# Kernel optimization log

Measured on AMD Instinct MI355X. Metric: run time of the kernel, lower is better.

Reference implementation:

```python
import jax, jax.numpy as jnp
import numpy as np

BN_EPS = 1e-5
NORM_EPS = 1e-12  # F.normalize default eps


def reference(x, conv_w, bn_gamma, bn_beta):
    # 1x1 conv dimension reduction: [B,2048,H,W] -> [B,256,H,W]
    z = jnp.einsum('bchw,dc->bdhw', x, conv_w)
    # BatchNorm2d (training-mode batch statistics) + ReLU
    mu = z.mean(axis=(0, 2, 3), keepdims=True)
    var = z.var(axis=(0, 2, 3), keepdims=True)
    z = (z - mu) / jnp.sqrt(var + BN_EPS)
    z = z * bn_gamma.reshape(1, -1, 1, 1) + bn_beta.reshape(1, -1, 1, 1)
    z = jax.nn.relu(z)

    B, d, h, w = z.shape
    M = h * w
    xm = z.reshape(B, d, M)
    # Covpool: y = x I_hat x^T with I_hat = (I - 11^T/M)/M == centered 2nd moment
    xc = xm - xm.mean(axis=-1, keepdims=True)
    cov = jnp.einsum('bdm,bem->bde', xc, xc) / M  # [B,d,d]

    # Eigen decomposition (cov is symmetric PSD; SVD of PSD == eigh)
    s, U = jnp.linalg.eigh(cov)  # s: [B,d], U: [B,d,d]
    eps = jnp.finfo(cov.dtype).eps
    s = jnp.maximum(s, eps)

    # ExponentialInverse: U exp(-S) U^T
    inv_x = jnp.einsum('bid,bd,bjd->bij', U, jnp.exp(-s), U)
    # Power (matrix sqrt): U S^{1/2} U^T
    out = jnp.einsum('bid,bd,bjd->bij', U, jnp.sqrt(s), U)

    # attention = out @ inv_x^T  (inv_x is symmetric, transpose kept for fidelity)
    att = jnp.einsum('bij,bkj->bik', out, inv_x)
    flat = att.reshape(B, -1)
    nrm = jnp.maximum(jnp.linalg.norm(flat, axis=1, keepdims=True), NORM_EPS)
    normalized = (flat / nrm).reshape(att.shape)
    att = out * (att / normalized)

    y = att + out
    iu = jnp.triu_indices(d)
    return y[:, iu[0], iu[1]]  # [B, d*(d+1)/2]


def setup_inputs() -> dict:
    key = jax.random.key(0)
    k1, k2 = jax.random.split(key)
    x = jax.random.normal(k1, (32, 2048, 28, 28), dtype=jnp.float32)
    # kaiming-normal fan_out scaling for 1x1 conv: std = sqrt(2/fan_out)=sqrt(2/256)
    conv_w = jax.random.normal(k2, (256, 2048), dtype=jnp.float32) * np.sqrt(2.0 / 256.0)
    bn_gamma = jnp.ones((256,), dtype=jnp.float32)
    bn_beta = jnp.zeros((256,), dtype=jnp.float32)
    return {'x': x, 'conv_w': conv_w, 'bn_gamma': bn_gamma, 'bn_beta': bn_beta}
```

## Files before the change

kernel.cpp:

```cpp
#include <hip/hip_runtime.h>


typedef unsigned short u16;
typedef __attribute__((ext_vector_type(8))) short bf16x8;
typedef __attribute__((ext_vector_type(4))) float f32x4;

__device__ __forceinline__ u16 f2bf(float f) {
  unsigned u = __builtin_bit_cast(unsigned, f);
  u += 0x7FFFu + ((u >> 16) & 1u);
  return (u16)(u >> 16);
}
__device__ __forceinline__ float bf2f(u16 h) {
  unsigned u = ((unsigned)h) << 16;
  return __builtin_bit_cast(float, u);
}

__device__ __forceinline__
void mm_core(const u16* __restrict__ Ah, const u16* __restrict__ Al,
             const u16* __restrict__ Bh, const u16* __restrict__ Bl,
             long boff, int row0, int col0,
             u16 (*lds)[128][8][8], f32x4 acc[4][4])
{
  const int tid = threadIdx.x;
  const int wave = tid >> 6, lane = tid & 63;
  const int wm = wave >> 1, wn = wave & 1;
  const int mL = lane & 15, q = lane >> 4;
  const u16* baseA[2] = {Ah + boff, Al + boff};
  const u16* baseB[2] = {Bh + boff, Bl + boff};

  for (int k0 = 0; k0 < 256; k0 += 64) {
    __syncthreads();
#pragma unroll
    for (int it = 0; it < 16; ++it) {
      const int t = it >> 2;
      const int r = ((it & 3) << 8) + tid;
      const int m = r >> 3, c = r & 7;
      const u16* src = (t < 2 ? baseA[t] : baseB[t - 2])
                     + (long)((t < 2 ? row0 : col0) + m) * 256 + k0 + c * 8;
      const uint4 v = *reinterpret_cast<const uint4*>(src);
      *reinterpret_cast<uint4*>(&lds[t][m][c ^ (m & 7)][0]) = v;
    }
    __syncthreads();
#pragma unroll
    for (int kk = 0; kk < 2; ++kk) {
      bf16x8 ah[4], al[4], bh[4], bl[4];
#pragma unroll
      for (int i = 0; i < 4; ++i) {
        const int ma = wm * 64 + i * 16 + mL;
        const int ca = (kk * 4 + q) ^ (ma & 7);
        ah[i] = *reinterpret_cast<const bf16x8*>(&lds[0][ma][ca][0]);
        al[i] = *reinterpret_cast<const bf16x8*>(&lds[1][ma][ca][0]);
        const int nb = wn * 64 + i * 16 + mL;
        const int cb = (kk * 4 + q) ^ (nb & 7);
        bh[i] = *reinterpret_cast<const bf16x8*>(&lds[2][nb][cb][0]);
        bl[i] = *reinterpret_cast<const bf16x8*>(&lds[3][nb][cb][0]);
      }
#pragma unroll
      for (int i = 0; i < 4; ++i)
#pragma unroll
        for (int j = 0; j < 4; ++j) {
          acc[i][j] = __builtin_amdgcn_mfma_f32_16x16x32_bf16(ah[i], bh[j], acc[i][j], 0, 0, 0);
          acc[i][j] = __builtin_amdgcn_mfma_f32_16x16x32_bf16(ah[i], bl[j], acc[i][j], 0, 0, 0);
          acc[i][j] = __builtin_amdgcn_mfma_f32_16x16x32_bf16(al[i], bh[j], acc[i][j], 0, 0, 0);
        }
    }
  }
}

template<int MODE>
__global__ __launch_bounds__(256)
void gemm2_k(const u16* __restrict__ Ah, const u16* __restrict__ Al,
             const u16* __restrict__ Bh, const u16* __restrict__ Bl,
             u16* __restrict__ Ch, u16* __restrict__ Cl,
             u16* __restrict__ Dh, u16* __restrict__ Dl,
             const float* __restrict__ covf,
             float alpha, float b1, float diag, float* __restrict__ attn2)
{
  __shared__ u16 lds[4][128][8][8];
  const long boff = (long)blockIdx.z * 65536;
  const int row0 = blockIdx.y * 128, col0 = blockIdx.x * 128;
  const int wave = threadIdx.x >> 6, lane = threadIdx.x & 63;
  const int wm = wave >> 1, wn = wave & 1;
  const int mL = lane & 15, q = lane >> 4;

  f32x4 acc[4][4];
#pragma unroll
  for (int i = 0; i < 4; ++i)
#pragma unroll
    for (int j = 0; j < 4; ++j) acc[i][j] = {0.f, 0.f, 0.f, 0.f};

  mm_core(Ah, Al, Bh, Bl, boff, row0, col0, lds, acc);

  if (MODE == 2) {
    float ssum = 0.f;
#pragma unroll
    for (int i = 0; i < 4; ++i)
#pragma unroll
      for (int j = 0; j < 4; ++j)
#pragma unroll
        for (int rg = 0; rg < 4; ++rg) ssum = fmaf(acc[i][j][rg], acc[i][j][rg], ssum);
#pragma unroll
    for (int o = 32; o > 0; o >>= 1) ssum += __shfl_down(ssum, o);
    __syncthreads();
    float* red = (float*)&lds[0][0][0][0];
    if (lane == 0) red[wave] = ssum;
    __syncthreads();
    if (threadIdx.x == 0)
      atomicAdd(attn2 + blockIdx.z, red[0] + red[1] + red[2] + red[3]);
    return;
  }

#pragma unroll
  for (int i = 0; i < 4; ++i) {
    const int rbase = row0 + wm * 64 + i * 16 + q * 4;
#pragma unroll
    for (int j = 0; j < 4; ++j) {
      const int cc = col0 + wn * 64 + j * 16 + mL;
#pragma unroll
      for (int rg = 0; rg < 4; ++rg) {
        const int rr = rbase + rg;
        const long o = boff + (long)rr * 256 + cc;
        if (MODE == 0) {
          float v = alpha * acc[i][j][rg];
          if (covf) v = fmaf(b1, covf[o], v);
          if (rr == cc) v += diag;
          const u16 h = f2bf(v);
          Ch[o] = h; Cl[o] = f2bf(v - bf2f(h));
        } else {
          const float v = acc[i][j][rg];
          u16 h = f2bf(v);
          Ch[o] = h; Cl[o] = f2bf(v - bf2f(h));
          float hv = v * (1.f / 40320.f) - covf[o] * (1.f / 5040.f);
          if (rr == cc) hv += 1.f / 720.f;
          h = f2bf(hv);
          Dh[o] = h; Dl[o] = f2bf(hv - bf2f(h));
        }
      }
    }
  }
}

__global__ __launch_bounds__(256)
void gemm2_pair_k(const u16* __restrict__ A0, const u16* __restrict__ B0, u16* __restrict__ C0,
                  const u16* __restrict__ A1, const u16* __restrict__ B1, u16* __restrict__ C1,
                  long LO)
{
  __shared__ u16 lds[4][128][8][8];
  int z = blockIdx.z;
  const u16 *Ah, *Bh; u16* Chp;
  if (z < 32) { Ah = A0; Bh = B0; Chp = C0; }
  else { z -= 32; Ah = A1; Bh = B1; Chp = C1; }
  const long boff = (long)z * 65536;
  const int row0 = blockIdx.y * 128, col0 = blockIdx.x * 128;
  const int wave = threadIdx.x >> 6, lane = threadIdx.x & 63;
  const int wm = wave >> 1, wn = wave & 1;
  const int mL = lane & 15, q = lane >> 4;

  f32x4 acc[4][4];
#pragma unroll
  for (int i = 0; i < 4; ++i)
#pragma unroll
    for (int j = 0; j < 4; ++j) acc[i][j] = {0.f, 0.f, 0.f, 0.f};

  mm_core(Ah, Ah + LO, Bh, Bh + LO, boff, row0, col0, lds, acc);

#pragma unroll
  for (int i = 0; i < 4; ++i) {
    const int rbase = row0 + wm * 64 + i * 16 + q * 4;
#pragma unroll
    for (int j = 0; j < 4; ++j) {
      const int cc = col0 + wn * 64 + j * 16 + mL;
#pragma unroll
      for (int rg = 0; rg < 4; ++rg) {
        const long o = boff + (long)(rbase + rg) * 256 + cc;
        const float v = acc[i][j][rg];
        const u16 h = f2bf(v);
        Chp[o] = h; Chp[o + LO] = f2bf(v - bf2f(h));
      }
    }
  }
}

__global__ __launch_bounds__(512)
void conv_k(const u16* __restrict__ wb, const float* __restrict__ x,
            float* __restrict__ z)
{
  __shared__ u16 ldsA[256][8][8];
  __shared__ u16 ldsB[128][8][8];
  const int tid = threadIdx.x;
  const int b = blockIdx.z;
  const int n0 = blockIdx.x * 128;
  const int wave = tid >> 6, lane = tid & 63;
  const int wm = wave >> 1, wn = wave & 1;
  const int mL = lane & 15, q = lane >> 4;
  const float* xb = x + (long)b * 2048 * 784;

  f32x4 acc[4][4];
#pragma unroll
  for (int i = 0; i < 4; ++i)
#pragma unroll
    for (int j = 0; j < 4; ++j) acc[i][j] = {0.f, 0.f, 0.f, 0.f};

  for (int k0 = 0; k0 < 2048; k0 += 64) {
    __syncthreads();
#pragma unroll
    for (int it = 0; it < 4; ++it) {
      const int g = it * 512 + tid;
      const int m = g >> 3, c = g & 7;
      const uint4 v = *reinterpret_cast<const uint4*>(wb + (long)m * 2048 + k0 + c * 8);
      *reinterpret_cast<uint4*>(&ldsA[m][c ^ (m & 7)][0]) = v;
    }
    {
      const int kg = tid >> 5, nc = tid & 31;
      const int kbase = kg * 4, nbase = nc * 4;
      float vv[4][4];
#pragma unroll
      for (int jk = 0; jk < 4; ++jk) {
        const int gk = k0 + kbase + jk;
        const int gn = n0 + nbase;
        float4 f = make_float4(0.f, 0.f, 0.f, 0.f);
        if (gn < 784) f = *reinterpret_cast<const float4*>(xb + (long)gk * 784 + gn);
        vv[jk][0] = f.x; vv[jk][1] = f.y; vv[jk][2] = f.z; vv[jk][3] = f.w;
      }
      const int c = kbase >> 3, ko = kbase & 7;
#pragma unroll
      for (int jn = 0; jn < 4; ++jn) {
        const int n = nbase + jn;
        ushort4 u;
        u.x = f2bf(vv[0][jn]); u.y = f2bf(vv[1][jn]);
        u.z = f2bf(vv[2][jn]); u.w = f2bf(vv[3][jn]);
        *reinterpret_cast<ushort4*>(&ldsB[n][c ^ (n & 7)][ko]) = u;
      }
    }
    __syncthreads();
#pragma unroll
    for (int kk = 0; kk < 2; ++kk) {
      bf16x8 af[4], bfv[4];
#pragma unroll
      for (int i = 0; i < 4; ++i) {
        const int ma = wm * 64 + i * 16 + mL;
        af[i] = *reinterpret_cast<const bf16x8*>(&ldsA[ma][(kk * 4 + q) ^ (ma & 7)][0]);
        const int nb = wn * 64 + i * 16 + mL;
        bfv[i] = *reinterpret_cast<const bf16x8*>(&ldsB[nb][(kk * 4 + q) ^ (nb & 7)][0]);
      }
#pragma unroll
      for (int i = 0; i < 4; ++i)
#pragma unroll
        for (int j = 0; j < 4; ++j)
          acc[i][j] = __builtin_amdgcn_mfma_f32_16x16x32_bf16(af[i], bfv[j], acc[i][j], 0, 0, 0);
    }
  }
#pragma unroll
  for (int i = 0; i < 4; ++i) {
    const int rbase = wm * 64 + i * 16 + q * 4;
#pragma unroll
    for (int j = 0; j < 4; ++j) {
      const int cc = n0 + wn * 64 + j * 16 + mL;
      if (cc >= 784) continue;
#pragma unroll
      for (int rg = 0; rg < 4; ++rg)
        z[((long)b * 256 + rbase + rg) * 784 + cc] = acc[i][j][rg];
    }
  }
}

__global__ __launch_bounds__(256)
void gram_k(const u16* __restrict__ zb, const float* __restrict__ rs,
            float* __restrict__ cov)
{
  __shared__ u16 lds[2][128][8][8];
  const int tid = threadIdx.x;
  const int b = blockIdx.z;
  const int col0 = blockIdx.x * 128, row0 = blockIdx.y * 128;
  const int wave = tid >> 6, lane = tid & 63;
  const int wm = wave >> 1, wn = wave & 1;
  const int mL = lane & 15, q = lane >> 4;
  const u16* zbb = zb + (long)b * 256 * 832;

  f32x4 acc[4][4];
#pragma unroll
  for (int i = 0; i < 4; ++i)
#pragma unroll
    for (int j = 0; j < 4; ++j) acc[i][j] = {0.f, 0.f, 0.f, 0.f};

  for (int k0 = 0; k0 < 832; k0 += 64) {
    __syncthreads();
#pragma unroll
    for (int it = 0; it < 8; ++it) {
      const int t = it >> 2;
      const int r = ((it & 3) << 8) + tid;
      const int m = r >> 3, c = r & 7;
      const int grow = (t == 0 ? row0 : col0) + m;
      const uint4 v = *reinterpret_cast<const uint4*>(zbb + (long)grow * 832 + k0 + c * 8);
      *reinterpret_cast<uint4*>(&lds[t][m][c ^ (m & 7)][0]) = v;
    }
    __syncthreads();
#pragma unroll
    for (int kk = 0; kk < 2; ++kk) {
      bf16x8 af[4], bfv[4];
#pragma unroll
      for (int i = 0; i < 4; ++i) {
        const int ma = wm * 64 + i * 16 + mL;
        af[i] = *reinterpret_cast<const bf16x8*>(&lds[0][ma][(kk * 4 + q) ^ (ma & 7)][0]);
        const int nb = wn * 64 + i * 16 + mL;
        bfv[i] = *reinterpret_cast<const bf16x8*>(&lds[1][nb][(kk * 4 + q) ^ (nb & 7)][0]);
      }
#pragma unroll
      for (int i = 0; i < 4; ++i)
#pragma unroll
        for (int j = 0; j < 4; ++j)
          acc[i][j] = __builtin_amdgcn_mfma_f32_16x16x32_bf16(af[i], bfv[j], acc[i][j], 0, 0, 0);
    }
  }
  const float inv_m = 1.f / 784.f;
#pragma unroll
  for (int i = 0; i < 4; ++i) {
    const int rr0 = row0 + wm * 64 + i * 16 + q * 4;
#pragma unroll
    for (int j = 0; j < 4; ++j) {
      const int cc = col0 + wn * 64 + j * 16 + mL;
      const float mu_c = rs[b * 256 + cc] * inv_m;
#pragma unroll
      for (int rg = 0; rg < 4; ++rg) {
        const int rr = rr0 + rg;
        const float mu_r = rs[b * 256 + rr] * inv_m;
        cov[((long)b * 256 + rr) * 256 + cc] = fmaf(acc[i][j][rg], inv_m, -mu_r * mu_c);
      }
    }
  }
}

__global__ __launch_bounds__(256)
void bn_fuse_k(const float* __restrict__ z, const float* __restrict__ gamma,
               const float* __restrict__ beta, u16* __restrict__ zb,
               float* __restrict__ rs)
{
  const int d = blockIdx.x, t = threadIdx.x;
  const int lane = t & 63, wid = t >> 6;
  __shared__ float ws[4], wq[4], bc[2];

  float s = 0.f, qq = 0.f;
  for (int b = 0; b < 32; ++b) {
    const float* p = z + ((long)b * 256 + d) * 784;
    for (int m = t; m < 784; m += 256) {
      const float v = p[m];
      s += v; qq = fmaf(v, v, qq);
    }
  }
#pragma unroll
  for (int o = 32; o > 0; o >>= 1) { s += __shfl_down(s, o); qq += __shfl_down(qq, o); }
  if (lane == 0) { ws[wid] = s; wq[wid] = qq; }
  __syncthreads();
  if (t == 0) {
    const float inv_n = 1.f / 25088.f;
    const float sum = ws[0] + ws[1] + ws[2] + ws[3];
    const float sq  = wq[0] + wq[1] + wq[2] + wq[3];
    const float mean = sum * inv_n;
    const float var  = sq * inv_n - mean * mean;
    const float sc = gamma[d] * rsqrtf(var + 1e-5f);
    bc[0] = sc; bc[1] = fmaf(-mean, sc, beta[d]);
  }
  __syncthreads();
  const float sc = bc[0], sh = bc[1];

  for (int b = 0; b < 32; ++b) {
    const float* p = z + ((long)b * 256 + d) * 784;
    u16* qp = zb + ((long)b * 256 + d) * 832;
    float rsum = 0.f;
    for (int m = t; m < 832; m += 256) {
      const float v = (m < 784) ? fmaxf(fmaf(p[m], sc, sh), 0.f) : 0.f;
      qp[m] = f2bf(v);
      rsum += v;
    }
#pragma unroll
    for (int o = 32; o > 0; o >>= 1) rsum += __shfl_down(rsum, o);
    if (lane == 0) ws[wid] = rsum;
    __syncthreads();
    if (t == 0) rs[b * 256 + d] = ws[0] + ws[1] + ws[2] + ws[3];
    __syncthreads();
  }
}

__global__ __launch_bounds__(256)
void power_k(const float* __restrict__ cov, float* __restrict__ s,
             float* __restrict__ attn2)
{
  const int b = blockIdx.x, i = threadIdx.x;
  const float* A = cov + (long)b * 65536;
  __shared__ float v[256];
  __shared__ float red[4];
  v[i] = 1.f;
  __syncthreads();
  float lam = 1.f;
  for (int it = 0; it < 10; ++it) {
    float u = 0.f;
#pragma unroll 8
    for (int j = 0; j < 256; ++j) u = fmaf(A[(long)j * 256 + i], v[j], u);
    float ss = u * u;
#pragma unroll
    for (int o = 32; o > 0; o >>= 1) ss += __shfl_down(ss, o);
    if ((i & 63) == 0) red[i >> 6] = ss;
    __syncthreads();
    lam = sqrtf(red[0] + red[1] + red[2] + red[3]);
    v[i] = u / lam;
    __syncthreads();
  }
  if (i == 0) { s[b] = 1.8f / lam; attn2[b] = 0.f; }
}

__global__ __launch_bounds__(256)
void init_k(const float* __restrict__ cov, const float* __restrict__ s,
            u16* __restrict__ Yh, u16* __restrict__ Yl,
            u16* __restrict__ Th, u16* __restrict__ Tl)
{
  const int b = blockIdx.y, i = blockIdx.x, j = threadIdx.x;
  const long o = ((long)b * 256 + i) * 256 + j;
  const float a = cov[o] * s[b];
  u16 h = f2bf(a);
  Yh[o] = h; Yl[o] = f2bf(a - bf2f(h));
  float tv = -0.5f * a;
  if (i == j) tv += 1.5f;
  h = f2bf(tv);
  Th[o] = h; Tl[o] = f2bf(tv - bf2f(h));
}

__global__ __launch_bounds__(256)
void split_cov_k(const float* __restrict__ cov, u16* __restrict__ Ch, u16* __restrict__ Cl)
{
  const int b = blockIdx.y, i = blockIdx.x, j = threadIdx.x;
  const long o = ((long)b * 256 + i) * 256 + j;
  const float a = cov[o];
  const u16 h = f2bf(a);
  Ch[o] = h; Cl[o] = f2bf(a - bf2f(h));
}

__global__ __launch_bounds__(256)
void out_k(const u16* __restrict__ Yh, const u16* __restrict__ Yl,
           const float* __restrict__ s, const float* __restrict__ attn2,
           float* __restrict__ out)
{
  const int i = blockIdx.x, b = blockIdx.y, j = threadIdx.x;
  if (j < i) return;
  const float inv = rsqrtf(s[b]);
  const float nrm = fmaxf(sqrtf(fmaxf(attn2[b], 0.f)) * inv, 1e-12f);
  const float scv = inv * (1.f + nrm);
  const long o = ((long)b * 256 + i) * 256 + j;
  const long off = (long)b * 32896 + (long)i * 256 - (long)i * (i - 1) / 2 + (j - i);
  out[off] = (bf2f(Yh[o]) + bf2f(Yl[o])) * scv;
}

__global__ __launch_bounds__(256)
void cast_w_k(const float* __restrict__ w, u16* __restrict__ wb)
{
  const int idx = blockIdx.x * 256 + threadIdx.x;
  wb[idx] = f2bf(w[idx]);
}

extern "C" void kernel_launch(void* const* d_in, const int* in_sizes, int n_in,
                              void* d_out, int out_size, void* d_ws, size_t ws_size,
                              hipStream_t stream)
{
  const float* x     = (const float*)d_in[0];
  const float* w     = (const float*)d_in[1];
  const float* gamma = (const float*)d_in[2];
  const float* beta  = (const float*)d_in[3];
  float* out = (float*)d_out;

  const long PS = 4194304;
  const long LO = 2097152;
  u16* S[5];
  for (int k = 0; k < 5; ++k) S[k] = (u16*)d_ws + (long)k * PS;
  float* z   = (float*)d_ws;
  u16*   zb  = (u16*)((char*)d_ws + 25690112);
  float* cov = (float*)((char*)d_ws + 41943040);
  u16*   wb  = (u16*)((char*)d_ws + 41943040);
  float* st  = (float*)((char*)d_ws + 50331648);
  float* sv = st, *attn2 = st + 32, *rs = st + 64;

  const dim3 blk(256);
  const dim3 gM(2, 2, 32);
  const dim3 gP(2, 2, 64);
  const dim3 gE(256, 32);

  auto G0 = [&](const u16* A_, const u16* B_, u16* C_, const float* Pf,
                float alpha, float b1, float diag) {
    gemm2_k<0><<<gM, blk, 0, stream>>>(A_, A_ + LO, B_, B_ + LO, C_, C_ + LO,
                                       (u16*)nullptr, (u16*)nullptr, Pf,
                                       alpha, b1, diag, (float*)nullptr);
  };

  cast_w_k<<<dim3(2048), blk, 0, stream>>>(w, wb);
  conv_k<<<dim3(7, 1, 32), dim3(512), 0, stream>>>(wb, x, z);
  bn_fuse_k<<<dim3(256), blk, 0, stream>>>(z, gamma, beta, zb, rs);
  gram_k<<<gM, blk, 0, stream>>>(zb, rs, cov);
  power_k<<<dim3(32), blk, 0, stream>>>(cov, sv, attn2);
  init_k<<<gE, blk, 0, stream>>>(cov, sv, S[0], S[0] + LO, S[1], S[1] + LO);
  G0(S[0], S[1], S[2], nullptr, 1.f, 0.f, 0.f);

  int iY = 2, iZ = 1, fa = 0, fb = 3, fc = 4;
  for (int it = 1; it <= 7; ++it) {
    const int iT = fa;
    G0(S[iZ], S[iY], S[iT], nullptr, -0.5f, 0.f, 1.5f);
    if (it < 7) {
      gemm2_pair_k<<<gP, blk, 0, stream>>>(S[iY], S[iT], S[fb],
                                           S[iT], S[iZ], S[fc], LO);
      const int nY = fb, nZ = fc;
      fa = iY; fb = iZ; fc = iT;
      iY = nY; iZ = nZ;
    } else {
      G0(S[iY], S[iT], S[fb], nullptr, 1.f, 0.f, 0.f);
      iY = fb;
    }
  }
  int fr[4], nf = 0;
  for (int k = 0; k < 5; ++k) if (k != iY) fr[nf++] = k;
  u16* C2 = S[fr[0]]; u16* V = S[fr[1]]; u16* Ha = S[fr[2]]; u16* Hb = S[fr[3]];

  split_cov_k<<<gE, blk, 0, stream>>>(cov, C2, C2 + LO);
  gemm2_k<1><<<gM, blk, 0, stream>>>(C2, C2 + LO, C2, C2 + LO, V, V + LO,
                                     Ha, Ha + LO, cov, 1.f, 0.f, 0.f, (float*)nullptr);
  G0(V, Ha, Hb, cov, 1.f, -1.f / 120.f, 1.f / 24.f);
  G0(V, Hb, Ha, cov, 1.f, -1.f / 6.f,   0.5f);
  G0(V, Ha, Hb, cov, 1.f, -1.f,         1.f);

  gemm2_k<2><<<gM, blk, 0, stream>>>(S[iY], S[iY] + LO, Hb, Hb + LO,
                                     (u16*)nullptr, (u16*)nullptr,
                                     (u16*)nullptr, (u16*)nullptr,
                                     (const float*)nullptr, 1.f, 0.f, 0.f, attn2);
  out_k<<<gE, blk, 0, stream>>>(S[iY], S[iY] + LO, sv, attn2, out);
}
```

Before: 819.4 us.

## Co-schedule exp-polynomial GEMMs with Newton-Schulz steps and split BN into parallel kernels

Moves the Taylor-series matrix-exponential GEMM chain into the same launches as the first Newton-Schulz iterations, so independent 32-batch GEMMs share one 64-block grid instead of running as separate small grids. It also fuses the weight bf16 cast into the conv loader and the cov hi/lo split into the gram epilogue. BatchNorm is split into a stats kernel and an apply kernel with much wider grids. Remaining standalone GEMMs use a 128x64 tile to double the block count. The cost is extra workspace buffers and more launches in the BN path.

Result: faster. 776.2 us (-5.3%).

```diff
diff --git a/kernel.cpp b/kernel.cpp
--- a/kernel.cpp
+++ b/kernel.cpp
@@ -67,17 +67,22 @@
   }
 }
 
-template<int MODE>
-__global__ __launch_bounds__(256)
-void gemm2_k(const u16* __restrict__ Ah, const u16* __restrict__ Al,
-             const u16* __restrict__ Bh, const u16* __restrict__ Bl,
-             u16* __restrict__ Ch, u16* __restrict__ Cl,
-             u16* __restrict__ Dh, u16* __restrict__ Dl,
-             const float* __restrict__ covf,
-             float alpha, float b1, float diag, float* __restrict__ attn2)
+template<int MB>
+__global__ __launch_bounds__(256)
+void fuse_k(const u16* __restrict__ A0, const u16* __restrict__ B0, u16* __restrict__ C0,
+            float al0, float b10, float dg0, const float* __restrict__ cf0,
+            const u16* __restrict__ A1, const u16* __restrict__ B1, u16* __restrict__ C1,
+            u16* __restrict__ D1, float al1, float b11, float dg1,
+            float hc1, float hc2, float hc3, const float* __restrict__ cf1, long LO)
 {
   __shared__ u16 lds[4][128][8][8];
-  const long boff = (long)blockIdx.z * 65536;
+  int z = blockIdx.z;
+  const bool hB = (z >= 32);
+  const u16 *Ah, *Bh; u16 *C, *D = nullptr;
+  float al, b1, dg; const float* cf;
+  if (!hB) { Ah = A0; Bh = B0; C = C0; al = al0; b1 = b10; dg = dg0; cf = cf0; }
+  else { z -= 32; Ah = A1; Bh = B1; C = C1; D = D1; al = al1; b1 = b11; dg = dg1; cf = cf1; }
+  const long boff = (long)z * 65536;
   const int row0 = blockIdx.y * 128, col0 = blockIdx.x * 128;
   const int wave = threadIdx.x >> 6, lane = threadIdx.x & 63;
   const int wm = wave >> 1, wn = wave & 1;
@@ -89,26 +94,7 @@
 #pragma unroll
     for (int j = 0; j < 4; ++j) acc[i][j] = {0.f, 0.f, 0.f, 0.f};
 
-  mm_core(Ah, Al, Bh, Bl, boff, row0, col0, lds, acc);
-
-  if (MODE == 2) {
-    float ssum = 0.f;
-#pragma unroll
-    for (int i = 0; i < 4; ++i)
-#pragma unroll
-      for (int j = 0; j < 4; ++j)
-#pragma unroll
-        for (int rg = 0; rg < 4; ++rg) ssum = fmaf(acc[i][j][rg], acc[i][j][rg], ssum);
-#pragma unroll
-    for (int o = 32; o > 0; o >>= 1) ssum += __shfl_down(ssum, o);
-    __syncthreads();
-    float* red = (float*)&lds[0][0][0][0];
-    if (lane == 0) red[wave] = ssum;
-    __syncthreads();
-    if (threadIdx.x == 0)
-      atomicAdd(attn2 + blockIdx.z, red[0] + red[1] + red[2] + red[3]);
-    return;
-  }
+  mm_core(Ah, Ah + LO, Bh, Bh + LO, boff, row0, col0, lds, acc);
 
 #pragma unroll
   for (int i = 0; i < 4; ++i) {
@@ -120,20 +106,20 @@
       for (int rg = 0; rg < 4; ++rg) {
         const int rr = rbase + rg;
         const long o = boff + (long)rr * 256 + cc;
-        if (MODE == 0) {
-          float v = alpha * acc[i][j][rg];
-          if (covf) v = fmaf(b1, covf[o], v);
-          if (rr == cc) v += diag;
+        const float vr = acc[i][j][rg];
+        if (MB == 1 && hB) {
+          u16 h = f2bf(vr);
+          C[o] = h; C[o + LO] = f2bf(vr - bf2f(h));
+          float hv = fmaf(vr, hc1, cf[o] * hc2);
+          if (rr == cc) hv += hc3;
+          h = f2bf(hv);
+          D[o] = h; D[o + LO] = f2bf(hv - bf2f(h));
+        } else {
+          float v = al * vr;
+          if (cf) v = fmaf(b1, cf[o], v);
+          if (rr == cc) v += dg;
           const u16 h = f2bf(v);
-          Ch[o] = h; Cl[o] = f2bf(v - bf2f(h));
-        } else {
-          const float v = acc[i][j][rg];
-          u16 h = f2bf(v);
-          Ch[o] = h; Cl[o] = f2bf(v - bf2f(h));
-          float hv = v * (1.f / 40320.f) - covf[o] * (1.f / 5040.f);
-          if (rr == cc) hv += 1.f / 720.f;
-          h = f2bf(hv);
-          Dh[o] = h; Dl[o] = f2bf(hv - bf2f(h));
+          C[o] = h; C[o + LO] = f2bf(v - bf2f(h));
         }
       }
     }
@@ -181,8 +167,121 @@
   }
 }
 
+template<int MODE>
+__global__ __launch_bounds__(256)
+void gemmN64_k(const u16* __restrict__ Ah, const u16* __restrict__ Al,
+               const u16* __restrict__ Bh, const u16* __restrict__ Bl,
+               u16* __restrict__ Ch, u16* __restrict__ Cl,
+               const float* __restrict__ cf, float alpha, float b1, float diag,
+               float* __restrict__ attn2)
+{
+  __shared__ u16 ldsA[2][128][8][8];
+  __shared__ u16 ldsB[2][64][8][8];
+  const long boff = (long)blockIdx.z * 65536;
+  const int row0 = blockIdx.y * 128, col0 = blockIdx.x * 64;
+  const int tid = threadIdx.x;
+  const int wave = tid >> 6, lane = tid & 63;
+  const int wm = wave >> 1, wn = wave & 1;
+  const int mL = lane & 15, q = lane >> 4;
+  const u16* baseA[2] = {Ah + boff, Al + boff};
+  const u16* baseB[2] = {Bh + boff, Bl + boff};
+
+  f32x4 acc[4][2];
+#pragma unroll
+  for (int i = 0; i < 4; ++i)
+#pragma unroll
+    for (int j = 0; j < 2; ++j) acc[i][j] = {0.f, 0.f, 0.f, 0.f};
+
+  for (int k0 = 0; k0 < 256; k0 += 64) {
+    __syncthreads();
+#pragma unroll
+    for (int it = 0; it < 8; ++it) {
+      const int t = it >> 2;
+      const int r = ((it & 3) << 8) + tid;
+      const int m = r >> 3, c = r & 7;
+      const uint4 v = *reinterpret_cast<const uint4*>(
+          baseA[t] + (long)(row0 + m) * 256 + k0 + c * 8);
+      *reinterpret_cast<uint4*>(&ldsA[t][m][c ^ (m & 7)][0]) = v;
+    }
+#pragma unroll
+    for (int it = 0; it < 4; ++it) {
+      const int t = it >> 1;
+      const int r = ((it & 1) << 8) + tid;
+      const int m = r >> 3, c = r & 7;
+      const uint4 v = *reinterpret_cast<const uint4*>(
+          baseB[t] + (long)(col0 + m) * 256 + k0 + c * 8);
+      *reinterpret_cast<uint4*>(&ldsB[t][m][c ^ (m & 7)][0]) = v;
+    }
+    __syncthreads();
+#pragma unroll
+    for (int kk = 0; kk < 2; ++kk) {
+      bf16x8 ah[4], alo[4], bh[2], bl[2];
+#pragma unroll
+      for (int i = 0; i < 4; ++i) {
+        const int ma = wm * 64 + i * 16 + mL;
+        const int ca = (kk * 4 + q) ^ (ma & 7);
+        ah[i]  = *reinterpret_cast<const bf16x8*>(&ldsA[0][ma][ca][0]);
+        alo[i] = *reinterpret_cast<const bf16x8*>(&ldsA[1][ma][ca][0]);
+      }
+#pragma unroll
+      for (int j = 0; j < 2; ++j) {
+        const int nb = wn * 32 + j * 16 + mL;
+        const int cb = (kk * 4 + q) ^ (nb & 7);
+        bh[j] = *reinterpret_cast<const bf16x8*>(&ldsB[0][nb][cb][0]);
+        bl[j] = *reinterpret_cast<const bf16x8*>(&ldsB[1][nb][cb][0]);
+      }
+#pragma unroll
+      for (int i = 0; i < 4; ++i)
+#pragma unroll
+        for (int j = 0; j < 2; ++j) {
+          acc[i][j] = __builtin_amdgcn_mfma_f32_16x16x32_bf16(ah[i],  bh[j], acc[i][j], 0, 0, 0);
+          acc[i][j] = __builtin_amdgcn_mfma_f32_16x16x32_bf16(ah[i],  bl[j], acc[i][j], 0, 0, 0);
+          acc[i][j] = __builtin_amdgcn_mfma_f32_16x16x32_bf16(alo[i], bh[j], acc[i][j], 0, 0, 0);
+        }
+    }
+  }
+
+  if (MODE == 2) {
+    float ssum = 0.f;
+#pragma unroll
+    for (int i = 0; i < 4; ++i)
+#pragma unroll
+      for (int j = 0; j < 2; ++j)
+#pragma unroll
+        for (int rg = 0; rg < 4; ++rg) ssum = fmaf(acc[i][j][rg], acc[i][j][rg], ssum);
+#pragma unroll
+    for (int o = 32; o > 0; o >>= 1) ssum += __shfl_down(ssum, o);
+    __syncthreads();
+    float* red = (float*)&ldsA[0][0][0][0];
+    if (lane == 0) red[wave] = ssum;
+    __syncthreads();
+    if (tid == 0)
+      atomicAdd(attn2 + blockIdx.z, red[0] + red[1] + red[2] + red[3]);
+    return;
+  }
+
+#pragma unroll
+  for (int i = 0; i < 4; ++i) {
+    const int rbase = row0 + wm * 64 + i * 16 + q * 4;
+#pragma unroll
+    for (int j = 0; j < 2; ++j) {
+      const int cc = col0 + wn * 32 + j * 16 + mL;
+#pragma unroll
+      for (int rg = 0; rg < 4; ++rg) {
+        const int rr = rbase + rg;
+        const long o = boff + (long)rr * 256 + cc;
+        float v = alpha * acc[i][j][rg];
+        if (cf) v = fmaf(b1, cf[o], v);
+        if (rr == cc) v += diag;
+        const u16 h = f2bf(v);
+        Ch[o] = h; Cl[o] = f2bf(v - bf2f(h));
+      }
+    }
+  }
+}
+
 __global__ __launch_bounds__(512)
-void conv_k(const u16* __restrict__ wb, const float* __restrict__ x,
+void conv_k(const float* __restrict__ w, const float* __restrict__ x,
             float* __restrict__ z)
 {
   __shared__ u16 ldsA[256][8][8];
@@ -207,8 +306,13 @@
     for (int it = 0; it < 4; ++it) {
       const int g = it * 512 + tid;
       const int m = g >> 3, c = g & 7;
-      const uint4 v = *reinterpret_cast<const uint4*>(wb + (long)m * 2048 + k0 + c * 8);
-      *reinterpret_cast<uint4*>(&ldsA[m][c ^ (m & 7)][0]) = v;
+      const float4 f0 = *reinterpret_cast<const float4*>(w + (long)m * 2048 + k0 + c * 8);
+      const float4 f1 = *reinterpret_cast<const float4*>(w + (long)m * 2048 + k0 + c * 8 + 4);
+      ushort4 ua, ub;
+      ua.x = f2bf(f0.x); ua.y = f2bf(f0.y); ua.z = f2bf(f0.z); ua.w = f2bf(f0.w);
+      ub.x = f2bf(f1.x); ub.y = f2bf(f1.y); ub.z = f2bf(f1.z); ub.w = f2bf(f1.w);
+      *reinterpret_cast<ushort4*>(&ldsA[m][c ^ (m & 7)][0]) = ua;
+      *reinterpret_cast<ushort4*>(&ldsA[m][c ^ (m & 7)][4]) = ub;
     }
     {
       const int kg = tid >> 5, nc = tid & 31;
@@ -266,7 +370,7 @@
 
 __global__ __launch_bounds__(256)
 void gram_k(const u16* __restrict__ zb, const float* __restrict__ rs,
-            float* __restrict__ cov)
+            float* __restrict__ cov, u16* __restrict__ C2h, u16* __restrict__ C2l)
 {
   __shared__ u16 lds[2][128][8][8];
   const int tid = threadIdx.x;
@@ -324,23 +428,25 @@
       for (int rg = 0; rg < 4; ++rg) {
         const int rr = rr0 + rg;
         const float mu_r = rs[b * 256 + rr] * inv_m;
-        cov[((long)b * 256 + rr) * 256 + cc] = fmaf(acc[i][j][rg], inv_m, -mu_r * mu_c);
-      }
-    }
-  }
-}
-
-__global__ __launch_bounds__(256)
-void bn_fuse_k(const float* __restrict__ z, const float* __restrict__ gamma,
-               const float* __restrict__ beta, u16* __restrict__ zb,
-               float* __restrict__ rs)
-{
-  const int d = blockIdx.x, t = threadIdx.x;
+        const long o = ((long)b * 256 + rr) * 256 + cc;
+        const float cv = fmaf(acc[i][j][rg], inv_m, -mu_r * mu_c);
+        cov[o] = cv;
+        const u16 h = f2bf(cv);
+        C2h[o] = h; C2l[o] = f2bf(cv - bf2f(h));
+      }
+    }
+  }
+}
+
+__global__ __launch_bounds__(256)
+void bn_stats_k(const float* __restrict__ z, float* __restrict__ ps,
+                float* __restrict__ pq)
+{
+  const int d = blockIdx.x, sl = blockIdx.y, t = threadIdx.x;
   const int lane = t & 63, wid = t >> 6;
-  __shared__ float ws[4], wq[4], bc[2];
-
+  __shared__ float ws[4], wq[4];
   float s = 0.f, qq = 0.f;
-  for (int b = 0; b < 32; ++b) {
+  for (int b = sl * 4; b < sl * 4 + 4; ++b) {
     const float* p = z + ((long)b * 256 + d) * 784;
     for (int m = t; m < 784; m += 256) {
       const float v = p[m];
@@ -352,33 +458,45 @@
   if (lane == 0) { ws[wid] = s; wq[wid] = qq; }
   __syncthreads();
   if (t == 0) {
+    ps[d * 8 + sl] = ws[0] + ws[1] + ws[2] + ws[3];
+    pq[d * 8 + sl] = wq[0] + wq[1] + wq[2] + wq[3];
+  }
+}
+
+__global__ __launch_bounds__(256)
+void bn_apply_k(const float* __restrict__ z, const float* __restrict__ gamma,
+                const float* __restrict__ beta, const float* __restrict__ ps,
+                const float* __restrict__ pq, u16* __restrict__ zb,
+                float* __restrict__ rs)
+{
+  const int d = blockIdx.x, b = blockIdx.y, t = threadIdx.x;
+  const int lane = t & 63, wid = t >> 6;
+  __shared__ float bc[2], ws[4];
+  if (t == 0) {
+    float sum = 0.f, sq = 0.f;
+#pragma unroll
+    for (int s8 = 0; s8 < 8; ++s8) { sum += ps[d * 8 + s8]; sq += pq[d * 8 + s8]; }
     const float inv_n = 1.f / 25088.f;
-    const float sum = ws[0] + ws[1] + ws[2] + ws[3];
-    const float sq  = wq[0] + wq[1] + wq[2] + wq[3];
     const float mean = sum * inv_n;
-    const float var  = sq * inv_n - mean * mean;
+    const float var = sq * inv_n - mean * mean;
     const float sc = gamma[d] * rsqrtf(var + 1e-5f);
     bc[0] = sc; bc[1] = fmaf(-mean, sc, beta[d]);
   }
   __syncthreads();
   const float sc = bc[0], sh = bc[1];
-
-  for (int b = 0; b < 32; ++b) {
-    const float* p = z + ((long)b * 256 + d) * 784;
-    u16* qp = zb + ((long)b * 256 + d) * 832;
-    float rsum = 0.f;
-    for (int m = t; m < 832; m += 256) {
-      const float v = (m < 784) ? fmaxf(fmaf(p[m], sc, sh), 0.f) : 0.f;
-      qp[m] = f2bf(v);
-      rsum += v;
-    }
-#pragma unroll
-    for (int o = 32; o > 0; o >>= 1) rsum += __shfl_down(rsum, o);
-    if (lane == 0) ws[wid] = rsum;
-    __syncthreads();
-    if (t == 0) rs[b * 256 + d] = ws[0] + ws[1] + ws[2] + ws[3];
-    __syncthreads();
-  }
+  const float* p = z + ((long)b * 256 + d) * 784;
+  u16* qp = zb + ((long)b * 256 + d) * 832;
+  float rsum = 0.f;
+  for (int m = t; m < 832; m += 256) {
+    const float v = (m < 784) ? fmaxf(fmaf(p[m], sc, sh), 0.f) : 0.f;
+    qp[m] = f2bf(v);
+    rsum += v;
+  }
+#pragma unroll
+  for (int o = 32; o > 0; o >>= 1) rsum += __shfl_down(rsum, o);
+  if (lane == 0) ws[wid] = rsum;
+  __syncthreads();
+  if (t == 0) rs[b * 256 + d] = ws[0] + ws[1] + ws[2] + ws[3];
 }
 
 __global__ __launch_bounds__(256)
@@ -425,16 +543,6 @@
 }
 
 __global__ __launch_bounds__(256)
-void split_cov_k(const float* __restrict__ cov, u16* __restrict__ Ch, u16* __restrict__ Cl)
-{
-  const int b = blockIdx.y, i = blockIdx.x, j = threadIdx.x;
-  const long o = ((long)b * 256 + i) * 256 + j;
-  const float a = cov[o];
-  const u16 h = f2bf(a);
-  Ch[o] = h; Cl[o] = f2bf(a - bf2f(h));
-}
-
-__global__ __launch_bounds__(256)
 void out_k(const u16* __restrict__ Yh, const u16* __restrict__ Yl,
            const float* __restrict__ s, const float* __restrict__ attn2,
            float* __restrict__ out)
@@ -449,13 +557,6 @@
   out[off] = (bf2f(Yh[o]) + bf2f(Yl[o])) * scv;
 }
 
-__global__ __launch_bounds__(256)
-void cast_w_k(const float* __restrict__ w, u16* __restrict__ wb)
-{
-  const int idx = blockIdx.x * 256 + threadIdx.x;
-  wb[idx] = f2bf(w[idx]);
-}
-
 extern "C" void kernel_launch(void* const* d_in, const int* in_sizes, int n_in,
                               void* d_out, int out_size, void* d_ws, size_t ws_size,
                               hipStream_t stream)
@@ -468,39 +569,56 @@
 
   const long PS = 4194304;
   const long LO = 2097152;
-  u16* S[5];
-  for (int k = 0; k < 5; ++k) S[k] = (u16*)d_ws + (long)k * PS;
-  float* z   = (float*)d_ws;
-  u16*   zb  = (u16*)((char*)d_ws + 25690112);
-  float* cov = (float*)((char*)d_ws + 41943040);
-  u16*   wb  = (u16*)((char*)d_ws + 41943040);
-  float* st  = (float*)((char*)d_ws + 50331648);
+  u16* S[9];
+  for (int k = 0; k < 9; ++k) S[k] = (u16*)d_ws + (long)k * PS;
+  char* base = (char*)d_ws;
+  float* z   = (float*)(base + 75497472);
+  u16*   zb  = (u16*)(base + 101187584);
+  float* cov = (float*)(base + 114819072);
+  float* st  = (float*)(base + 123207680);
   float* sv = st, *attn2 = st + 32, *rs = st + 64;
+  float* ps = st + 64 + 8192, *pq = ps + 2048;
+  u16 *C2 = S[5], *V = S[6], *Ha = S[7], *Hb = S[8];
 
   const dim3 blk(256);
-  const dim3 gM(2, 2, 32);
   const dim3 gP(2, 2, 64);
+  const dim3 gT(4, 2, 32);
   const dim3 gE(256, 32);
 
-  auto G0 = [&](const u16* A_, const u16* B_, u16* C_, const float* Pf,
-                float alpha, float b1, float diag) {
-    gemm2_k<0><<<gM, blk, 0, stream>>>(A_, A_ + LO, B_, B_ + LO, C_, C_ + LO,
-                                       (u16*)nullptr, (u16*)nullptr, Pf,
-                                       alpha, b1, diag, (float*)nullptr);
-  };
-
-  cast_w_k<<<dim3(2048), blk, 0, stream>>>(w, wb);
-  conv_k<<<dim3(7, 1, 32), dim3(512), 0, stream>>>(wb, x, z);
-  bn_fuse_k<<<dim3(256), blk, 0, stream>>>(z, gamma, beta, zb, rs);
-  gram_k<<<gM, blk, 0, stream>>>(zb, rs, cov);
+  conv_k<<<dim3(7, 1, 32), dim3(512), 0, stream>>>(w, x, z);
+  bn_stats_k<<<dim3(256, 8), blk, 0, stream>>>(z, ps, pq);
+  bn_apply_k<<<dim3(256, 32), blk, 0, stream>>>(z, gamma, beta, ps, pq, zb, rs);
+  gram_k<<<dim3(2, 2, 32), blk, 0, stream>>>(zb, rs, cov, C2, C2 + LO);
   power_k<<<dim3(32), blk, 0, stream>>>(cov, sv, attn2);
   init_k<<<gE, blk, 0, stream>>>(cov, sv, S[0], S[0] + LO, S[1], S[1] + LO);
-  G0(S[0], S[1], S[2], nullptr, 1.f, 0.f, 0.f);
+
+  fuse_k<1><<<gP, blk, 0, stream>>>(
+      S[0], S[1], S[2], 1.f, 0.f, 0.f, (const float*)nullptr,
+      C2, C2, V, Ha, 1.f, 0.f, 0.f,
+      1.f / 40320.f, -1.f / 5040.f, 1.f / 720.f, cov, LO);
 
   int iY = 2, iZ = 1, fa = 0, fb = 3, fc = 4;
   for (int it = 1; it <= 7; ++it) {
     const int iT = fa;
-    G0(S[iZ], S[iY], S[iT], nullptr, -0.5f, 0.f, 1.5f);
+    if (it == 1)
+      fuse_k<0><<<gP, blk, 0, stream>>>(
+          S[iZ], S[iY], S[iT], -0.5f, 0.f, 1.5f, (const float*)nullptr,
+          V, Ha, Hb, (u16*)nullptr, 1.f, -1.f / 120.f, 1.f / 24.f,
+          0.f, 0.f, 0.f, cov, LO);
+    else if (it == 2)
+      fuse_k<0><<<gP, blk, 0, stream>>>(
+          S[iZ], S[iY], S[iT], -0.5f, 0.f, 1.5f, (const float*)nullptr,
+          V, Hb, Ha, (u16*)nullptr, 1.f, -1.f / 6.f, 0.5f,
+          0.f, 0.f, 0.f, cov, LO);
+    else if (it == 3)
+      fuse_k<0><<<gP, blk, 0, stream>>>(
+          S[iZ], S[iY], S[iT], -0.5f, 0.f, 1.5f, (const float*)nullptr,
+          V, Ha, Hb, (u16*)nullptr, 1.f, -1.f, 1.f,
+          0.f, 0.f, 0.f, cov, LO);
+    else
+      gemmN64_k<0><<<gT, blk, 0, stream>>>(
+          S[iZ], S[iZ] + LO, S[iY], S[iY] + LO, S[iT], S[iT] + LO,
+          (const float*)nullptr, -0.5f, 0.f, 1.5f, (float*)nullptr);
     if (it < 7) {
       gemm2_pair_k<<<gP, blk, 0, stream>>>(S[iY], S[iT], S[fb],
                                            S[iT], S[iZ], S[fc], LO);
@@ -508,24 +626,15 @@
       fa = iY; fb = iZ; fc = iT;
       iY = nY; iZ = nZ;
     } else {
-      G0(S[iY], S[iT], S[fb], nullptr, 1.f, 0.f, 0.f);
+      gemmN64_k<0><<<gT, blk, 0, stream>>>(
+          S[iY], S[iY] + LO, S[iT], S[iT] + LO, S[fb], S[fb] + LO,
+          (const float*)nullptr, 1.f, 0.f, 0.f, (float*)nullptr);
       iY = fb;
     }
   }
-  int fr[4], nf = 0;
-  for (int k = 0; k < 5; ++k) if (k != iY) fr[nf++] = k;
-  u16* C2 = S[fr[0]]; u16* V = S[fr[1]]; u16* Ha = S[fr[2]]; u16* Hb = S[fr[3]];
-
-  split_cov_k<<<gE, blk, 0, stream>>>(cov, C2, C2 + LO);
-  gemm2_k<1><<<gM, blk, 0, stream>>>(C2, C2 + LO, C2, C2 + LO, V, V + LO,
-                                     Ha, Ha + LO, cov, 1.f, 0.f, 0.f, (float*)nullptr);
-  G0(V, Ha, Hb, cov, 1.f, -1.f / 120.f, 1.f / 24.f);
-  G0(V, Hb, Ha, cov, 1.f, -1.f / 6.f,   0.5f);
-  G0(V, Ha, Hb, cov, 1.f, -1.f,         1.f);
-
-  gemm2_k<2><<<gM, blk, 0, stream>>>(S[iY], S[iY] + LO, Hb, Hb + LO,
-                                     (u16*)nullptr, (u16*)nullptr,
-                                     (u16*)nullptr, (u16*)nullptr,
-                                     (const float*)nullptr, 1.f, 0.f, 0.f, attn2);
+
+  gemmN64_k<2><<<gT, blk, 0, stream>>>(
+      S[iY], S[iY] + LO, Hb, Hb + LO, (u16*)nullptr, (u16*)nullptr,
+      (const float*)nullptr, 1.f, 0.f, 0.f, attn2);
   out_k<<<gE, blk, 0, stream>>>(S[iY], S[iY] + LO, sv, attn2, out);
 }
```
